# Performance work log

Measured on AMD Instinct MI355X. Metric: run time of the kernel, lower is better.

## Reference

```python
import jax, jax.numpy as jnp
import numpy as np
from jax import lax

B, H, W, C, K, R, CB = 2, 128, 128, 256, 64, 8, 256


def _conv(x, w, b=None, pad=1, lhs_dil=None, groups=1):
    out = lax.conv_general_dilated(x, w, (1, 1), [(pad, pad), (pad, pad)],
                                   lhs_dilation=lhs_dil, feature_group_count=groups,
                                   dimension_numbers=('NCHW', 'OIHW', 'NCHW'))
    return out if b is None else out + b[None, :, None, None]


def _silu(x):
    return x * jax.nn.sigmoid(x)


def _fuse(l0, l1, l2, p1w, p1b, p2w, p3w):
    # proj1: Conv(k=3)+SiLU (BN folded); proj2/proj3: grouped ConvTranspose2d as lhs-dilated grouped convs
    a = _silu(_conv(l0, p1w, p1b))
    b2 = _conv(l1, p2w, pad=2, lhs_dil=(2, 2), groups=CB)  # ConvT(2CB->CB, k4, s2, p1, g=CB)
    b3 = _conv(l2, p3w, pad=5, lhs_dil=(4, 4), groups=CB)  # ConvT(4CB->CB, k8, s4, p2, g=CB)
    return a + b2 + b3


def _corr_map(emb, trk):
    # emb: [H,W,C], trk: [K,C]; cosine-similarity correlation with local argmax radius masking
    e = emb / jnp.maximum(jnp.linalg.norm(emb, axis=-1, keepdims=True), 1e-12)
    t = trk / jnp.maximum(jnp.linalg.norm(trk, axis=-1, keepdims=True), 1e-12)
    y = jnp.maximum(jnp.einsum('hwc,kc->khw', e, t), 0.0)  # torch.where(y>0, y, 0)
    idx = jnp.argmax(y.reshape(K, -1), axis=1)             # first max, like torch.nonzero(...)[0]
    ai, aj = idx // W, idx % W
    rows = jnp.arange(H)[None, :, None]
    cols = jnp.arange(W)[None, None, :]
    m = ((rows >= (ai[:, None, None] - R)) & (rows < (ai[:, None, None] + R)) &
         (cols >= (aj[:, None, None] - R)) & (cols < (aj[:, None, None] + R)))
    s = jnp.sum(y * m, axis=0)
    return s / jnp.max(s)


def setup_inputs():
    key = jax.random.key(0)
    ks = jax.random.split(key, 32)
    r = lambda i, shp, s=0.02: jax.random.normal(ks[i], shp, jnp.float32) * s
    z = lambda n: jnp.zeros((n,), jnp.float32)
    return dict(
        id_embeding=jax.random.normal(ks[0], (B, H, W, C), jnp.float32),
        tracklets=jax.random.normal(ks[1], (B, K, C), jnp.float32),
        l0=jax.random.normal(ks[2], (B, CB, H, W), jnp.float32),
        l1=jax.random.normal(ks[3], (B, 2 * CB, H // 2, W // 2), jnp.float32),
        l2=jax.random.normal(ks[4], (B, 4 * CB, H // 4, W // 4), jnp.float32),
        b_p1w=r(5, (CB, CB, 3, 3)), b_p1b=z(CB),
        b_p2w=r(6, (CB, 2, 4, 4)), b_p3w=r(7, (CB, 4, 8, 8)),
        b_c1w=r(8, (CB, CB, 3, 3)), b_c1b=z(CB),
        b_c2w=r(9, (4, CB, 3, 3)), b_c2b=z(4),
        h_p1w=r(10, (CB, CB, 3, 3)), h_p1b=z(CB),
        h_p2w=r(11, (CB, 2, 4, 4)), h_p3w=r(12, (CB, 4, 8, 8)),
        h_c1aw=r(13, (CB, 1, 3, 3), 0.1), h_c1ab=z(CB),
        h_c1bw=r(14, (1, CB, 3, 3)), h_c1bb=z(1),
        h_c2aw=r(15, (CB, CB, 3, 3)), h_c2ab=z(CB),
        h_c2bw=r(16, (CB, CB, 3, 3)), h_c2bb=z(CB),
        h_c2cw=r(17, (1, CB, 3, 3)), h_c2cb=z(1),
    )


def reference(id_embeding, tracklets, l0, l1, l2,
              b_p1w, b_p1b, b_p2w, b_p3w, b_c1w, b_c1b, b_c2w, b_c2b,
              h_p1w, h_p1b, h_p2w, h_p3w,
              h_c1aw, h_c1ab, h_c1bw, h_c1bb,
              h_c2aw, h_c2ab, h_c2bw, h_c2bb, h_c2cw, h_c2cb):
    # correlation map per batch -> x_F [B,1,H,W]
    x_F = jax.vmap(_corr_map)(id_embeding, tracklets)[:, None]
    # recheck_Box head
    xd_box = _fuse(l0, l1, l2, b_p1w, b_p1b, b_p2w, b_p3w)
    xb = _silu(_conv(xd_box, b_c1w, b_c1b))
    siambox = jnp.transpose(_conv(xb, b_c2w, b_c2b), (0, 2, 3, 1))  # [B,H,W,4]
    # recheck_heatmap head
    xd_hm = _fuse(l0, l1, l2, h_p1w, h_p1b, h_p2w, h_p3w)
    xf = _conv(_silu(_conv(x_F, h_c1aw, h_c1ab)), h_c1bw, h_c1bb)   # [B,1,H,W]
    t = xf * xd_hm                                                  # broadcast over CB channels
    t = _silu(_conv(t, h_c2aw, h_c2ab))
    t = _silu(_conv(t, h_c2bw, h_c2bb))
    hmmap = jax.nn.sigmoid(_conv(t, h_c2cw, h_c2cb))                # [B,1,H,W]
    return (hmmap, siambox)
```

## Files before the change

kernel.cpp:

```cpp
#include <hip/hip_runtime.h>
#include <math.h>

#define HH 128
#define WW 128
#define HWSZ 16384
#define CC 256
#define KK 64
#define BB 2

typedef __bf16 bf16x8_t __attribute__((ext_vector_type(8)));
typedef float  f32x4_t  __attribute__((ext_vector_type(4)));

__device__ __forceinline__ float silu_f(float v) { return v / (1.f + expf(-v)); }
__device__ __forceinline__ float sigm_f(float v) { return 1.f / (1.f + expf(-v)); }

__device__ __forceinline__ float b2f(unsigned short u) {
    union { unsigned int i; float f; } x; x.i = ((unsigned int)u) << 16; return x.f;
}
__device__ __forceinline__ unsigned short f2b(float f) {
    union { float f; unsigned int i; } x; x.f = f;
    unsigned int r = x.i + 0x7FFFu + ((x.i >> 16) & 1u);
    return (unsigned short)(r >> 16);
}
__device__ __forceinline__ float u2f(unsigned int u) {
    union { unsigned int i; float f; } x; x.i = u; return x.f;
}

__global__ __launch_bounds__(256) void cvt_nhwc_kernel(const float* __restrict__ in,
                                                       unsigned short* __restrict__ out) {
    __shared__ float T[32][128];
    const int tid = threadIdx.x;
    const int y = blockIdx.x & 127;
    const int b = blockIdx.x >> 7;
    const float* inb = in + (size_t)b * CC * HWSZ + y * 128;
    unsigned short* outb = out + ((size_t)b * HWSZ + (size_t)y * 128) * CC;

    for (int c0 = 0; c0 < CC; c0 += 32) {
        __syncthreads();
        {
            int cl = tid >> 3;
            int xq = tid & 7;
            const float4* src = (const float4*)(inb + (size_t)(c0 + cl) * HWSZ);
            float4* dst = (float4*)&T[cl][0];
            #pragma unroll
            for (int j = 0; j < 4; j++) dst[xq * 4 + j] = src[xq * 4 + j];
        }
        __syncthreads();
        {
            int x = tid & 127, ch = tid >> 7;
            union { unsigned short u[16]; uint4 v[2]; } pk;
            #pragma unroll
            for (int j = 0; j < 16; j++) pk.u[j] = f2b(T[ch * 16 + j][x]);
            uint4* dst = (uint4*)&outb[(size_t)x * CC + c0 + ch * 16];
            dst[0] = pk.v[0];
            dst[1] = pk.v[1];
        }
    }
}

#define WTSZ (9 * 8 * 256 * 32)
__global__ __launch_bounds__(256) void wprep5_kernel(const float* __restrict__ w0,
                                                     const float* __restrict__ w1,
                                                     const float* __restrict__ w2,
                                                     const float* __restrict__ w3,
                                                     const float* __restrict__ w4,
                                                     unsigned short* __restrict__ wtbase) {
    const float* ws[5] = {w0, w1, w2, w3, w4};
    int set = blockIdx.y;
    const float* w = ws[set];
    int idx = blockIdx.x * 256 + threadIdx.x;
    int e   = idx & 7;
    int co  = (idx >> 3) & 255;
    int g   = (idx >> 11) & 3;
    int v   = idx >> 13;
    int cb  = v / 9;
    int t   = v - cb * 9;
    wtbase[(size_t)set * WTSZ + idx] = f2b(w[((size_t)co * 256 + cb * 32 + g * 8 + e) * 9 + t]);
}

#define EPAD 260
__global__ __launch_bounds__(256) void ycorr_kernel(const float* __restrict__ emb,
                                                    const float* __restrict__ trk,
                                                    float* __restrict__ y) {
    __shared__ __align__(16) float E[64 * EPAD];
    __shared__ __align__(16) float T[64 * EPAD];
    __shared__ float SE[64];
    __shared__ float ST[64];

    const int tid = threadIdx.x;
    const int b   = blockIdx.y;
    const int hw0 = blockIdx.x * 64;

    const float4* esrc = (const float4*)(emb + ((size_t)b * HWSZ + hw0) * CC);
    #pragma unroll
    for (int i = 0; i < 16; i++) {
        int q  = tid + i * 256;
        int px = q >> 6, c4 = q & 63;
        *(float4*)&E[px * EPAD + c4 * 4] = esrc[(size_t)px * 64 + c4];
    }
    const float4* tsrc = (const float4*)(trk + (size_t)b * KK * CC);
    #pragma unroll
    for (int i = 0; i < 16; i++) {
        int q = tid + i * 256;
        int k = q >> 6, c4 = q & 63;
        *(float4*)&T[k * EPAD + c4 * 4] = tsrc[(size_t)k * 64 + c4];
    }
    __syncthreads();

    if (tid < 64) {
        float ss = 0.f;
        const float4* ep = (const float4*)&E[tid * EPAD];
        #pragma unroll 8
        for (int c4 = 0; c4 < 64; c4++) {
            float4 v = ep[c4];
            ss += v.x * v.x + v.y * v.y + v.z * v.z + v.w * v.w;
        }
        SE[tid] = 1.f / fmaxf(sqrtf(ss), 1e-12f);
    } else if (tid < 128) {
        float ss = 0.f;
        const float4* tp = (const float4*)&T[(tid - 64) * EPAD];
        #pragma unroll 8
        for (int c4 = 0; c4 < 64; c4++) {
            float4 v = tp[c4];
            ss += v.x * v.x + v.y * v.y + v.z * v.z + v.w * v.w;
        }
        ST[tid - 64] = 1.f / fmaxf(sqrtf(ss), 1e-12f);
    }
    __syncthreads();

    const int pg = tid & 15;
    const int kg = tid >> 4;

    float acc[4][4];
    #pragma unroll
    for (int jp = 0; jp < 4; jp++)
        #pragma unroll
        for (int jk = 0; jk < 4; jk++) acc[jp][jk] = 0.f;

    const float* Ep[4];
    const float* Tp[4];
    #pragma unroll
    for (int jp = 0; jp < 4; jp++) Ep[jp] = &E[(jp * 16 + pg) * EPAD];
    #pragma unroll
    for (int jk = 0; jk < 4; jk++) Tp[jk] = &T[(jk * 16 + kg) * EPAD];

    #pragma unroll 2
    for (int c4 = 0; c4 < 64; ++c4) {
        float4 e[4], t[4];
        #pragma unroll
        for (int jp = 0; jp < 4; jp++) e[jp] = *(const float4*)(Ep[jp] + c4 * 4);
        #pragma unroll
        for (int jk = 0; jk < 4; jk++) t[jk] = *(const float4*)(Tp[jk] + c4 * 4);
        #define DOT4(a, t) (fmaf(a.w, t.w, fmaf(a.z, t.z, fmaf(a.y, t.y, a.x * t.x))))
        #pragma unroll
        for (int jp = 0; jp < 4; jp++)
            #pragma unroll
            for (int jk = 0; jk < 4; jk++)
                acc[jp][jk] += DOT4(e[jp], t[jk]);
        #undef DOT4
    }

    #pragma unroll
    for (int jp = 0; jp < 4; jp++) {
        int px = jp * 16 + pg;
        float se = SE[px];
        #pragma unroll
        for (int jk = 0; jk < 4; jk++) {
            int k = jk * 16 + kg;
            y[((size_t)b * KK + k) * HWSZ + hw0 + px] = fmaxf(acc[jp][jk], 0.f) * se * ST[k];
        }
    }
}

__global__ __launch_bounds__(256) void argmax_kernel(const float* __restrict__ y,
                                                     int* __restrict__ idxout,
                                                     unsigned int* __restrict__ umax) {
    int bk = blockIdx.x;
    int t = threadIdx.x;
    if (bk == 0 && t < BB) umax[t] = 0u;
    const float* p = y + (size_t)bk * HWSZ;
    float best = -1.f; int bi = 1 << 30;
    for (int i = t; i < HWSZ; i += 256) {
        float v = p[i];
        if (v > best) { best = v; bi = i; }
    }
    __shared__ float sv[256];
    __shared__ int   si[256];
    sv[t] = best; si[t] = bi;
    __syncthreads();
    for (int s = 128; s > 0; s >>= 1) {
        if (t < s) {
            float v2 = sv[t + s]; int i2 = si[t + s];
            if (v2 > sv[t] || (v2 == sv[t] && i2 < si[t])) { sv[t] = v2; si[t] = i2; }
        }
        __syncthreads();
    }
    if (t == 0) idxout[bk] = si[0];
}

__global__ __launch_bounds__(256) void smap_kernel(const float* __restrict__ y,
                                                   const int* __restrict__ idx,
                                                   float* __restrict__ s,
                                                   unsigned int* __restrict__ umax) {
    int b  = blockIdx.y;
    int hw = blockIdx.x * 256 + threadIdx.x;
    int h  = hw >> 7, w = hw & 127;
    __shared__ int ai[KK], aj[KK];
    if (threadIdx.x < KK) {
        int v = idx[b * KK + threadIdx.x];
        ai[threadIdx.x] = v >> 7;
        aj[threadIdx.x] = v & 127;
    }
    __syncthreads();
    const float* yb = y + (size_t)b * KK * HWSZ;
    float acc = 0.f;
    #pragma unroll 8
    for (int k = 0; k < KK; k++) {
        float v = yb[(size_t)k * HWSZ + hw];
        bool in = (h >= ai[k] - 8) && (h < ai[k] + 8) && (w >= aj[k] - 8) && (w < aj[k] + 8);
        acc += in ? v : 0.f;
    }
    s[(size_t)b * HWSZ + hw] = acc;

    __shared__ float sm[256];
    sm[threadIdx.x] = acc;
    __syncthreads();
    for (int st = 128; st > 0; st >>= 1) {
        if (threadIdx.x < st) sm[threadIdx.x] = fmaxf(sm[threadIdx.x], sm[threadIdx.x + st]);
        __syncthreads();
    }
    if (threadIdx.x == 0) {
        union { float f; unsigned int i; } x; x.f = sm[0];
        atomicMax(&umax[b], x.i);
    }
}

__global__ __launch_bounds__(256) void deconv_kernel(const float* __restrict__ l1,
                                                     const float* __restrict__ l2,
                                                     const float* __restrict__ w2,
                                                     const float* __restrict__ w3,
                                                     unsigned short* __restrict__ out) {
    __shared__ float L1[2][64][64];
    __shared__ float L2[4][32][32];

    const int tid = threadIdx.x;
    const int g   = blockIdx.x & 255;
    const int b   = blockIdx.x >> 8;

    const float4* l1b = (const float4*)(l1 + ((size_t)b * 2 * CC + 2 * g) * 4096);
    float4* L1p = (float4*)&L1[0][0][0];
    #pragma unroll
    for (int i = 0; i < 8; i++) L1p[tid + i * 256] = l1b[tid + i * 256];
    const float4* l2b = (const float4*)(l2 + ((size_t)b * 4 * CC + 4 * g) * 1024);
    float4* L2p = (float4*)&L2[0][0][0];
    #pragma unroll
    for (int i = 0; i < 4; i++) L2p[tid + i * 256] = l2b[tid + i * 256];

    const int x    = tid & 127;
    const int ytop = tid >> 7;
    const float* w2g = w2 + (size_t)g * 32;
    const float* w3g = w3 + (size_t)g * 256;

    const int pxo = x & 1, pyo = ytop & 1;
    const int mx0 = (x + pxo - 2) >> 1;
    const int dy2 = (ytop + pyo - 2) >> 1;
    const bool nok0 = (unsigned)mx0 < 64u;
    const bool nok1 = (unsigned)(mx0 + 1) < 64u;
    const int nc0 = mx0 & 63, nc1 = (mx0 + 1) & 63;
    float W2[2][2][2];
    #pragma unroll
    for (int ci = 0; ci < 2; ci++)
        #pragma unroll
        for (int a = 0; a < 2; a++)
            #pragma unroll
            for (int c = 0; c < 2; c++)
                W2[ci][a][c] = w2g[ci * 16 + (pyo + 2 * a) * 4 + (pxo + 2 * c)];

    const int px3 = (5 - (x & 3)) & 3;
    const int n30 = (x + px3 - 5) >> 2;
    const bool n3ok0 = (unsigned)n30 < 32u;
    const bool n3ok1 = (unsigned)(n30 + 1) < 32u;
    const int n3c0 = n30 & 31, n3c1 = (n30 + 1) & 31;
    int dy3[2];
    float W3[2][4][2][2];
    #pragma unroll
    for (int ph = 0; ph < 2; ph++) {
        int py3 = (5 - ((ytop + 2 * ph) & 3)) & 3;
        dy3[ph] = (2 * ph + ytop + py3 - 5) >> 2;
        #pragma unroll
        for (int ci = 0; ci < 4; ci++)
            #pragma unroll
            for (int a = 0; a < 2; a++)
                #pragma unroll
                for (int c = 0; c < 2; c++)
                    W3[ph][ci][a][c] = w3g[ci * 64 + (py3 + 4 * a) * 8 + (px3 + 4 * c)];
    }

    __syncthreads();

    unsigned short* outb = out + ((size_t)b * CC + g) * HWSZ;

    #pragma unroll 2
    for (int ii = 0; ii < 32; ++ii) {
        #pragma unroll
        for (int ph = 0; ph < 2; ph++) {
            const int i = 2 * ii + ph;
            float acc = 0.f;
            {
                const int m0 = i + dy2;
                #pragma unroll
                for (int a = 0; a < 2; a++) {
                    int m = m0 + a;
                    bool mok = (unsigned)m < 64u;
                    int mc = m & 63;
                    #pragma unroll
                    for (int ci = 0; ci < 2; ci++) {
                        float v0 = (mok && nok0) ? L1[ci][mc][nc0] : 0.f;
                        float v1 = (mok && nok1) ? L1[ci][mc][nc1] : 0.f;
                        acc = fmaf(W2[ci][a][0], v0, acc);
                        acc = fmaf(W2[ci][a][1], v1, acc);
                    }
                }
            }
            {
                const int m0 = ii + dy3[ph];
                #pragma unroll
                for (int a = 0; a < 2; a++) {
                    int m = m0 + a;
                    bool mok = (unsigned)m < 32u;
                    int mc = m & 31;
                    #pragma unroll
                    for (int ci = 0; ci < 4; ci++) {
                        float v0 = (mok && n3ok0) ? L2[ci][mc][n3c0] : 0.f;
                        float v1 = (mok && n3ok1) ? L2[ci][mc][n3c1] : 0.f;
                        acc = fmaf(W3[ph][ci][a][0], v0, acc);
                        acc = fmaf(W3[ph][ci][a][1], v1, acc);
                    }
                }
            }
            outb[(size_t)i * 256 + tid] = f2b(acc);
        }
    }
}

template <int ADDB, int MULF>
__global__ __launch_bounds__(256, 2) void conv_mfma_kernel(
    const unsigned short* __restrict__ in,
    const unsigned short* __restrict__ wt,
    const float* __restrict__ bias,
    const unsigned short* __restrict__ addb,
    const float* __restrict__ xf,
    unsigned short* __restrict__ out)
{
    __shared__ __align__(16) unsigned short Alds[2][3 * 130 * 32];

    const int tid  = threadIdx.x;
    const int lane = tid & 63;
    const int wv   = tid >> 6;
    const int wco  = wv >> 1;
    const int wpx  = wv & 1;
    const int l15  = lane & 15;
    const int kg   = lane >> 4;

    const int l   = (blockIdx.x & 7) * 64 + (blockIdx.x >> 3);
    const int y0  = l >> 2;
    const int co0 = ((l >> 1) & 1) * 128;
    const int b   = l & 1;

    const unsigned short* inb = in + (size_t)b * HWSZ * CC;
    const float* xfb = MULF ? (xf + (size_t)b * HWSZ) : nullptr;
    const unsigned short* wp = wt + (size_t)kg * 2048 + (size_t)(co0 + wco * 64 + l15) * 8;

    int ach[3][4];
    #pragma unroll
    for (int tl = 0; tl < 3; tl++)
        #pragma unroll
        for (int f = 0; f < 4; f++) {
            int px = wpx * 64 + f * 16 + l15 + tl;
            ach[tl][f] = (px * 4 + (kg ^ ((px >> 1) & 3))) * 8;
        }

    f32x4_t acc[4][4];
    #pragma unroll
    for (int i = 0; i < 4; i++)
        #pragma unroll
        for (int j = 0; j < 4; j++)
            acc[i][j] = (f32x4_t){0.f, 0.f, 0.f, 0.f};

    if (tid < 48) {
        int q4 = tid & 3;
        int hp = (tid >> 2) & 1;
        int r  = (tid >> 3) % 3;
        int bi = tid / 24;
        int px = hp ? 129 : 0;
        int chunk = (r * 130 + px) * 4 + (q4 ^ ((px >> 1) & 3));
        *reinterpret_cast<uint4*>(&Alds[bi][chunk * 8]) = make_uint4(0u, 0u, 0u, 0u);
    }

    uint4 streg[6];
    float sxf[6];

    auto load_A = [&](int cb) {
        #pragma unroll
        for (int i = 0; i < 6; i++) {
            int q   = tid + i * 256;
            int q4  = q & 3;
            int pxi = (q >> 2) & 127;
            int r   = q >> 9;
            int gy  = y0 - 1 + r;
            uint4 v = make_uint4(0u, 0u, 0u, 0u);
            float fxv = 0.f;
            if ((unsigned)gy < 128u) {
                v = *reinterpret_cast<const uint4*>(
                        inb + ((size_t)(gy * 128 + pxi)) * CC + cb * 32 + q4 * 8);
                if (MULF) fxv = xfb[gy * 128 + pxi];
            }
            streg[i] = v;
            if (MULF) sxf[i] = fxv;
        }
    };
    auto write_A = [&](int bufi) {
        #pragma unroll
        for (int i = 0; i < 6; i++) {
            int q   = tid + i * 256;
            int q4  = q & 3;
            int pxi = (q >> 2) & 127;
            int r   = q >> 9;
            int px  = pxi + 1;
            int chunk = (r * 130 + px) * 4 + (q4 ^ ((px >> 1) & 3));
            uint4 v = streg[i];
            if (MULF) {
                union { unsigned short u[8]; uint4 w; } pk;
                pk.w = v;
                float fm = sxf[i];
                #pragma unroll
                for (int e = 0; e < 8; e++) pk.u[e] = f2b(b2f(pk.u[e]) * fm);
                v = pk.w;
            }
            *reinterpret_cast<uint4*>(&Alds[bufi][chunk * 8]) = v;
        }
    };

    load_A(0);
    write_A(0);

    bf16x8_t W[3][4], P[2][4];
    #pragma unroll
    for (int f = 0; f < 4; f++) W[0][f] = *reinterpret_cast<const bf16x8_t*>(wp + f * 128);
    #pragma unroll
    for (int f = 0; f < 4; f++) W[1][f] = *reinterpret_cast<const bf16x8_t*>(wp + 8192 + f * 128);

    __syncthreads();
    #pragma unroll
    for (int f = 0; f < 4; f++)
        P[0][f] = *reinterpret_cast<const bf16x8_t*>(&Alds[0][ach[0][f]]);

    for (int cb = 0; cb < 8; ++cb) {
        const int bufi = cb & 1;
        if (cb + 1 < 8) load_A(cb + 1);
        const unsigned short* wcb = wp + (size_t)cb * 73728;
        #pragma unroll
        for (int t = 0; t < 9; ++t) {
            if (cb < 7 || t < 7) {
                #pragma unroll
                for (int f = 0; f < 4; f++)
                    W[(t + 2) % 3][f] = *reinterpret_cast<const bf16x8_t*>(
                        wcb + (t + 2) * 8192 + f * 128);
            }
            if (t < 8) {
                const int aoff = ((t + 1) / 3) * 4160;
                #pragma unroll
                for (int f = 0; f < 4; f++)
                    P[(t + 1) & 1][f] = *reinterpret_cast<const bf16x8_t*>(
                        &Alds[bufi][aoff + ach[(t + 1) % 3][f]]);
            }
            __builtin_amdgcn_sched_barrier(0);
            #pragma unroll
            for (int cf = 0; cf < 4; cf++)
                #pragma unroll
                for (int pf = 0; pf < 4; pf++)
                    acc[cf][pf] = __builtin_amdgcn_mfma_f32_16x16x32_bf16(
                        W[t % 3][cf], P[t & 1][pf], acc[cf][pf], 0, 0, 0);
        }
        if (cb + 1 < 8) write_A(bufi ^ 1);
        __syncthreads();
        if (cb + 1 < 8) {
            #pragma unroll
            for (int f = 0; f < 4; f++)
                P[0][f] = *reinterpret_cast<const bf16x8_t*>(&Alds[(cb + 1) & 1][ach[0][f]]);
        }
    }

    size_t outB = ((size_t)b * HWSZ + (size_t)y0 * 128) * CC;
    #pragma unroll
    for (int cf = 0; cf < 4; cf++) {
        int co = co0 + wco * 64 + cf * 16 + kg * 4;
        float bs0 = bias[co], bs1 = bias[co + 1], bs2 = bias[co + 2], bs3 = bias[co + 3];
        #pragma unroll
        for (int pf = 0; pf < 4; pf++) {
            int x = wpx * 64 + pf * 16 + l15;
            float v0 = silu_f(acc[cf][pf][0] + bs0);
            float v1 = silu_f(acc[cf][pf][1] + bs1);
            float v2 = silu_f(acc[cf][pf][2] + bs2);
            float v3 = silu_f(acc[cf][pf][3] + bs3);
            if (ADDB) {
                size_t ab = ((size_t)b * CC + co) * HWSZ + (size_t)y0 * 128 + x;
                v0 += b2f(addb[ab]);
                v1 += b2f(addb[ab + HWSZ]);
                v2 += b2f(addb[ab + 2 * HWSZ]);
                v3 += b2f(addb[ab + 3 * HWSZ]);
            }
            union { unsigned short u[4]; uint2 v; } pk;
            pk.u[0] = f2b(v0); pk.u[1] = f2b(v1); pk.u[2] = f2b(v2); pk.u[3] = f2b(v3);
            *reinterpret_cast<uint2*>(&out[outB + (size_t)x * CC + co]) = pk.v;
        }
    }
}

__global__ __launch_bounds__(256) void conv_c1a_kernel(const float* __restrict__ s,
                                                       const unsigned int* __restrict__ umax,
                                                       const float* __restrict__ w,
                                                       const float* __restrict__ bias,
                                                       unsigned short* __restrict__ out) {
    __shared__ float W[2304];
    __shared__ float S[3][34];

    const int tid = threadIdx.x;
    const int idx = blockIdx.x;
    const int b   = idx >> 9;
    const int seg = idx & 511;
    const int y   = seg >> 2;
    const int x0  = (seg & 3) * 32;

    for (int i = tid; i < 2304; i += 256) W[i] = w[i];
    if (tid < 102) {
        int r = tid / 34, xx = tid - r * 34;
        int gy = y - 1 + r, gx = x0 - 1 + xx;
        S[r][xx] = ((unsigned)gy < 128u && (unsigned)gx < 128u)
                       ? s[(size_t)b * HWSZ + gy * 128 + gx] : 0.f;
    }
    __syncthreads();

    const float im = 1.f / u2f(umax[b]);
    const int cog = tid >> 5;
    const int px  = tid & 31;

    float sv[9];
    #pragma unroll
    for (int r = 0; r < 3; r++)
        #pragma unroll
        for (int d = 0; d < 3; d++)
            sv[r * 3 + d] = S[r][px + d];

    unsigned short* op =
        &out[((size_t)b * HWSZ + (size_t)y * 128 + x0 + px) * CC + cog * 32];
    #pragma unroll
    for (int q = 0; q < 4; q++) {
        union { unsigned short u[8]; uint4 v; } pk;
        #pragma unroll
        for (int j = 0; j < 8; j++) {
            int co = cog * 32 + q * 8 + j;
            float a = 0.f;
            #pragma unroll
            for (int t = 0; t < 9; t++) a = fmaf(W[co * 9 + t], sv[t], a);
            pk.u[j] = f2b(silu_f(a * im + bias[co]));
        }
        *reinterpret_cast<uint4*>(op + q * 8) = pk.v;
    }
}

template <int COUT, int MODE>
__global__ __launch_bounds__(256) void small_conv_kernel(
    const unsigned short* __restrict__ in,
    const float* __restrict__ w,
    const float* __restrict__ bias,
    float* __restrict__ out)
{
    __shared__ float WL[COUT * 9 * 32 * 12];

    const int tid = threadIdx.x;
    for (int i = tid; i < COUT * 2304; i += 256) {
        int e = i & 7;
        int g = (i >> 3) & 31;
        int rest = i >> 8;
        int t = rest % 9;
        int co = rest / 9;
        WL[((co * 9 + t) * 32 + g) * 12 + e] = w[((size_t)co * 256 + g * 8 + e) * 9 + t];
    }
    __syncthreads();

    const int lane = tid & 63;
    const int wv   = tid >> 6;
    const int c32  = lane & 31;
    const int ps   = lane >> 5;
    const int grp  = blockIdx.x * 4 + wv;
    const int base = grp * 4;
    const int b    = base >> 14;
    const int pix  = base & (HWSZ - 1);
    const int y    = pix >> 7;
    const int x0   = pix & 127;
    const int p0x  = x0 + 2 * ps;

    const unsigned short* inb = in + (size_t)b * HWSZ * CC;

    uint4 d[3][4];
    #pragma unroll
    for (int r = 0; r < 3; r++) {
        int gy = y - 1 + r;
        #pragma unroll
        for (int cx = 0; cx < 4; cx++) {
            int gx = p0x - 1 + cx;
            uint4 v = make_uint4(0u, 0u, 0u, 0u);
            if ((unsigned)gy < 128u && (unsigned)gx < 128u)
                v = *reinterpret_cast<const uint4*>(
                        inb + ((size_t)(gy * 128 + gx)) * CC + c32 * 8);
            d[r][cx] = v;
        }
    }

    float acc[2][COUT];
    #pragma unroll
    for (int p = 0; p < 2; p++)
        #pragma unroll
        for (int c = 0; c < COUT; c++) acc[p][c] = 0.f;

    #pragma unroll
    for (int r = 0; r < 3; r++) {
        float f[4][8];
        #pragma unroll
        for (int cx = 0; cx < 4; cx++) {
            union { unsigned short u[8]; uint4 v; } pk;
            pk.v = d[r][cx];
            #pragma unroll
            for (int e = 0; e < 8; e++) f[cx][e] = b2f(pk.u[e]);
        }
        #pragma unroll
        for (int dx = 0; dx < 3; dx++) {
            #pragma unroll
            for (int co = 0; co < COUT; co++) {
                int bse = ((co * 9 + r * 3 + dx) * 32 + c32) * 12;
                float4 wa = *(const float4*)&WL[bse];
                float4 wb = *(const float4*)&WL[bse + 4];
                #pragma unroll
                for (int p = 0; p < 2; p++) {
                    const float* ff = f[dx + p];
                    float a = acc[p][co];
                    a = fmaf(ff[0], wa.x, a); a = fmaf(ff[1], wa.y, a);
                    a = fmaf(ff[2], wa.z, a); a = fmaf(ff[3], wa.w, a);
                    a = fmaf(ff[4], wb.x, a); a = fmaf(ff[5], wb.y, a);
                    a = fmaf(ff[6], wb.z, a); a = fmaf(ff[7], wb.w, a);
                    acc[p][co] = a;
                }
            }
        }
    }

    #pragma unroll
    for (int m = 1; m <= 16; m <<= 1)
        #pragma unroll
        for (int p = 0; p < 2; p++)
            #pragma unroll
            for (int co = 0; co < COUT; co++)
                acc[p][co] += __shfl_xor(acc[p][co], m);

    if (c32 == 0) {
        #pragma unroll
        for (int p = 0; p < 2; p++) {
            size_t pixidx = (size_t)base + 2 * ps + p;
            if (MODE == 0) {
                ((float4*)out)[pixidx] = make_float4(
                    acc[p][0] + bias[0],
                    acc[p][COUT > 1 ? 1 : 0] + bias[COUT > 1 ? 1 : 0],
                    acc[p][COUT > 2 ? 2 : 0] + bias[COUT > 2 ? 2 : 0],
                    acc[p][COUT > 3 ? 3 : 0] + bias[COUT > 3 ? 3 : 0]);
            } else if (MODE == 1) {
                out[pixidx] = acc[p][0] + bias[0];
            } else {
                out[pixidx] = sigm_f(acc[p][0] + bias[0]);
            }
        }
    }
}

extern "C" void kernel_launch(void* const* d_in, const int* in_sizes, int n_in,
                              void* d_out, int out_size, void* d_ws, size_t ws_size,
                              hipStream_t stream) {
    const float* emb    = (const float*)d_in[0];
    const float* trk    = (const float*)d_in[1];
    const float* l0     = (const float*)d_in[2];
    const float* l1     = (const float*)d_in[3];
    const float* l2     = (const float*)d_in[4];
    const float* b_p1w  = (const float*)d_in[5];
    const float* b_p1b  = (const float*)d_in[6];
    const float* b_p2w  = (const float*)d_in[7];
    const float* b_p3w  = (const float*)d_in[8];
    const float* b_c1w  = (const float*)d_in[9];
    const float* b_c1b  = (const float*)d_in[10];
    const float* b_c2w  = (const float*)d_in[11];
    const float* b_c2b  = (const float*)d_in[12];
    const float* h_p1w  = (const float*)d_in[13];
    const float* h_p1b  = (const float*)d_in[14];
    const float* h_p2w  = (const float*)d_in[15];
    const float* h_p3w  = (const float*)d_in[16];
    const float* h_c1aw = (const float*)d_in[17];
    const float* h_c1ab = (const float*)d_in[18];
    const float* h_c1bw = (const float*)d_in[19];
    const float* h_c1bb = (const float*)d_in[20];
    const float* h_c2aw = (const float*)d_in[21];
    const float* h_c2ab = (const float*)d_in[22];
    const float* h_c2bw = (const float*)d_in[23];
    const float* h_c2bb = (const float*)d_in[24];
    const float* h_c2cw = (const float*)d_in[25];
    const float* h_c2cb = (const float*)d_in[26];

    float* outp = (float*)d_out;

    const size_t ACT = (size_t)BB * CC * HWSZ;
    const size_t WT  = (size_t)WTSZ;

    unsigned short* l0nh = (unsigned short*)d_ws;
    unsigned short* wt0  = l0nh + ACT;
    unsigned short* wt1  = wt0 + WT;
    unsigned short* wt2  = wt1 + WT;
    unsigned short* wt3  = wt2 + WT;
    unsigned short* wt4  = wt3 + WT;
    unsigned short* Db   = wt4 + WT;
    unsigned short* X1   = Db + ACT;
    unsigned short* X2   = X1 + ACT;
    float* sbuf   = (float*)(X2 + ACT);
    float* xfb    = sbuf + (size_t)BB * HWSZ;
    unsigned int* umax = (unsigned int*)(xfb + (size_t)BB * HWSZ);
    int*   idxb   = (int*)(umax + 2);
    float* ybuf   = (float*)X1;

    cvt_nhwc_kernel<<<BB * 128, 256, 0, stream>>>(l0, l0nh);
    wprep5_kernel<<<dim3((unsigned)(WT / 256), 5), 256, 0, stream>>>(
        b_p1w, b_c1w, h_p1w, h_c2aw, h_c2bw, wt0);

    ycorr_kernel<<<dim3(256, BB), 256, 0, stream>>>(emb, trk, ybuf);
    argmax_kernel<<<BB * KK, 256, 0, stream>>>(ybuf, idxb, umax);
    smap_kernel<<<dim3(64, BB), 256, 0, stream>>>(ybuf, idxb, sbuf, umax);

    deconv_kernel<<<BB * CC, 256, 0, stream>>>(l1, l2, b_p2w, b_p3w, Db);
    conv_mfma_kernel<1, 0><<<512, 256, 0, stream>>>(l0nh, wt0, b_p1b, Db, nullptr, X1);
    conv_mfma_kernel<0, 0><<<512, 256, 0, stream>>>(X1, wt1, b_c1b, nullptr, nullptr, X2);
    small_conv_kernel<4, 0><<<2048, 256, 0, stream>>>(X2, b_c2w, b_c2b, outp + BB * HWSZ);

    deconv_kernel<<<BB * CC, 256, 0, stream>>>(l1, l2, h_p2w, h_p3w, Db);
    conv_mfma_kernel<1, 0><<<512, 256, 0, stream>>>(l0nh, wt2, h_p1b, Db, nullptr, X1);
    conv_c1a_kernel<<<1024, 256, 0, stream>>>(sbuf, umax, h_c1aw, h_c1ab, X2);
    small_conv_kernel<1, 1><<<2048, 256, 0, stream>>>(X2, h_c1bw, h_c1bb, xfb);
    conv_mfma_kernel<0, 1><<<512, 256, 0, stream>>>(X1, wt3, h_c2ab, nullptr, xfb, Db);
    conv_mfma_kernel<0, 0><<<512, 256, 0, stream>>>(Db, wt4, h_c2bb, nullptr, nullptr, X1);
    small_conv_kernel<1, 2><<<2048, 256, 0, stream>>>(X1, h_c2cw, h_c2cb, outp);
}
```

Baseline: 409.5 us.

## Merge both heads' deconv and proj1 conv into dual-head kernels sharing loaded inputs

The deconv kernel now computes both the box and heatmap heads' transposed convolutions from a single shared-memory load of l1/l2. The first 3x3 MFMA conv for both heads is merged into one 1024-block launch that reads l0 once and picks weights by head. This drops two launches, avoids reloading inputs, and gives the merged conv a larger grid. It needs an extra activation buffer in the workspace, and a fallback path keeps the old sequence when the workspace is too small.

```diff
diff --git a/kernel.cpp b/kernel.cpp
--- a/kernel.cpp
+++ b/kernel.cpp
@@ -235,11 +235,15 @@
     }
 }
 
+template <int HEADS>
 __global__ __launch_bounds__(256) void deconv_kernel(const float* __restrict__ l1,
                                                      const float* __restrict__ l2,
-                                                     const float* __restrict__ w2,
-                                                     const float* __restrict__ w3,
-                                                     unsigned short* __restrict__ out) {
+                                                     const float* __restrict__ w2a,
+                                                     const float* __restrict__ w3a,
+                                                     const float* __restrict__ w2b,
+                                                     const float* __restrict__ w3b,
+                                                     unsigned short* __restrict__ outA,
+                                                     unsigned short* __restrict__ outB) {
     __shared__ float L1[2][64][64];
     __shared__ float L2[4][32][32];
 
@@ -258,8 +262,6 @@
 
     const int x    = tid & 127;
     const int ytop = tid >> 7;
-    const float* w2g = w2 + (size_t)g * 32;
-    const float* w3g = w3 + (size_t)g * 256;
 
     const int pxo = x & 1, pyo = ytop & 1;
     const int mx0 = (x + pxo - 2) >> 1;
@@ -267,93 +269,107 @@
     const bool nok0 = (unsigned)mx0 < 64u;
     const bool nok1 = (unsigned)(mx0 + 1) < 64u;
     const int nc0 = mx0 & 63, nc1 = (mx0 + 1) & 63;
-    float W2[2][2][2];
-    #pragma unroll
-    for (int ci = 0; ci < 2; ci++)
-        #pragma unroll
-        for (int a = 0; a < 2; a++)
-            #pragma unroll
-            for (int c = 0; c < 2; c++)
-                W2[ci][a][c] = w2g[ci * 16 + (pyo + 2 * a) * 4 + (pxo + 2 * c)];
 
     const int px3 = (5 - (x & 3)) & 3;
     const int n30 = (x + px3 - 5) >> 2;
     const bool n3ok0 = (unsigned)n30 < 32u;
     const bool n3ok1 = (unsigned)(n30 + 1) < 32u;
     const int n3c0 = n30 & 31, n3c1 = (n30 + 1) & 31;
-    int dy3[2];
-    float W3[2][4][2][2];
+    int dy3[2], py3v[2];
     #pragma unroll
     for (int ph = 0; ph < 2; ph++) {
         int py3 = (5 - ((ytop + 2 * ph) & 3)) & 3;
+        py3v[ph] = py3;
         dy3[ph] = (2 * ph + ytop + py3 - 5) >> 2;
-        #pragma unroll
-        for (int ci = 0; ci < 4; ci++)
+    }
+
+    __syncthreads();
+
+    const float* w2s[2] = {w2a, w2b};
+    const float* w3s[2] = {w3a, w3b};
+    unsigned short* outs[2] = {outA, outB};
+
+    #pragma unroll 1
+    for (int hd = 0; hd < HEADS; ++hd) {
+        const float* w2g = w2s[hd] + (size_t)g * 32;
+        const float* w3g = w3s[hd] + (size_t)g * 256;
+
+        float W2[2][2][2];
+        #pragma unroll
+        for (int ci = 0; ci < 2; ci++)
             #pragma unroll
             for (int a = 0; a < 2; a++)
                 #pragma unroll
                 for (int c = 0; c < 2; c++)
-                    W3[ph][ci][a][c] = w3g[ci * 64 + (py3 + 4 * a) * 8 + (px3 + 4 * c)];
-    }
-
-    __syncthreads();
-
-    unsigned short* outb = out + ((size_t)b * CC + g) * HWSZ;
-
-    #pragma unroll 2
-    for (int ii = 0; ii < 32; ++ii) {
-        #pragma unroll
-        for (int ph = 0; ph < 2; ph++) {
-            const int i = 2 * ii + ph;
-            float acc = 0.f;
-            {
-                const int m0 = i + dy2;
+                    W2[ci][a][c] = w2g[ci * 16 + (pyo + 2 * a) * 4 + (pxo + 2 * c)];
+        float W3[2][4][2][2];
+        #pragma unroll
+        for (int ph = 0; ph < 2; ph++)
+            #pragma unroll
+            for (int ci = 0; ci < 4; ci++)
                 #pragma unroll
-                for (int a = 0; a < 2; a++) {
-                    int m = m0 + a;
-                    bool mok = (unsigned)m < 64u;
-                    int mc = m & 63;
+                for (int a = 0; a < 2; a++)
                     #pragma unroll
-                    for (int ci = 0; ci < 2; ci++) {
-                        float v0 = (mok && nok0) ? L1[ci][mc][nc0] : 0.f;
-                        float v1 = (mok && nok1) ? L1[ci][mc][nc1] : 0.f;
-                        acc = fmaf(W2[ci][a][0], v0, acc);
-                        acc = fmaf(W2[ci][a][1], v1, acc);
+                    for (int c = 0; c < 2; c++)
+                        W3[ph][ci][a][c] = w3g[ci * 64 + (py3v[ph] + 4 * a) * 8 + (px3 + 4 * c)];
+
+        unsigned short* outb = outs[hd] + ((size_t)b * CC + g) * HWSZ;
+
+        #pragma unroll 2
+        for (int ii = 0; ii < 32; ++ii) {
+            #pragma unroll
+            for (int ph = 0; ph < 2; ph++) {
+                const int i = 2 * ii + ph;
+                float acc = 0.f;
+                {
+                    const int m0 = i + dy2;
+                    #pragma unroll
+                    for (int a = 0; a < 2; a++) {
+                        int m = m0 + a;
+                        bool mok = (unsigned)m < 64u;
+                        int mc = m & 63;
+                        #pragma unroll
+                        for (int ci = 0; ci < 2; ci++) {
+                            float v0 = (mok && nok0) ? L1[ci][mc][nc0] : 0.f;
+                            float v1 = (mok && nok1) ? L1[ci][mc][nc1] : 0.f;
+                            acc = fmaf(W2[ci][a][0], v0, acc);
+                            acc = fmaf(W2[ci][a][1], v1, acc);
+                        }
                     }
                 }
-            }
-            {
-                const int m0 = ii + dy3[ph];
-                #pragma unroll
-                for (int a = 0; a < 2; a++) {
-                    int m = m0 + a;
-                    bool mok = (unsigned)m < 32u;
-                    int mc = m & 31;
+                {
+                    const int m0 = ii + dy3[ph];
                     #pragma unroll
-                    for (int ci = 0; ci < 4; ci++) {
-                        float v0 = (mok && n3ok0) ? L2[ci][mc][n3c0] : 0.f;
-                        float v1 = (mok && n3ok1) ? L2[ci][mc][n3c1] : 0.f;
-                        acc = fmaf(W3[ph][ci][a][0], v0, acc);
-                        acc = fmaf(W3[ph][ci][a][1], v1, acc);
+                    for (int a = 0; a < 2; a++) {
+                        int m = m0 + a;
+                        bool mok = (unsigned)m < 32u;
+                        int mc = m & 31;
+                        #pragma unroll
+                        for (int ci = 0; ci < 4; ci++) {
+                            float v0 = (mok && n3ok0) ? L2[ci][mc][n3c0] : 0.f;
+                            float v1 = (mok && n3ok1) ? L2[ci][mc][n3c1] : 0.f;
+                            acc = fmaf(W3[ph][ci][a][0], v0, acc);
+                            acc = fmaf(W3[ph][ci][a][1], v1, acc);
+                        }
                     }
                 }
+                outb[(size_t)i * 256 + tid] = f2b(acc);
             }
-            outb[(size_t)i * 256 + tid] = f2b(acc);
         }
     }
 }
 
 template <int ADDB, int MULF>
-__global__ __launch_bounds__(256, 2) void conv_mfma_kernel(
+__device__ __forceinline__ void conv_mfma_body(
+    int y0, int co0, int b,
     const unsigned short* __restrict__ in,
     const unsigned short* __restrict__ wt,
     const float* __restrict__ bias,
     const unsigned short* __restrict__ addb,
     const float* __restrict__ xf,
-    unsigned short* __restrict__ out)
+    unsigned short* __restrict__ out,
+    unsigned short (*Alds)[3 * 130 * 32])
 {
-    __shared__ __align__(16) unsigned short Alds[2][3 * 130 * 32];
-
     const int tid  = threadIdx.x;
     const int lane = tid & 63;
     const int wv   = tid >> 6;
@@ -361,11 +377,6 @@
     const int wpx  = wv & 1;
     const int l15  = lane & 15;
     const int kg   = lane >> 4;
-
-    const int l   = (blockIdx.x & 7) * 64 + (blockIdx.x >> 3);
-    const int y0  = l >> 2;
-    const int co0 = ((l >> 1) & 1) * 128;
-    const int b   = l & 1;
 
     const unsigned short* inb = in + (size_t)b * HWSZ * CC;
     const float* xfb = MULF ? (xf + (size_t)b * HWSZ) : nullptr;
@@ -515,6 +526,50 @@
             *reinterpret_cast<uint2*>(&out[outB + (size_t)x * CC + co]) = pk.v;
         }
     }
+}
+
+template <int ADDB, int MULF>
+__global__ __launch_bounds__(256, 2) void conv_mfma_kernel(
+    const unsigned short* __restrict__ in,
+    const unsigned short* __restrict__ wt,
+    const float* __restrict__ bias,
+    const unsigned short* __restrict__ addb,
+    const float* __restrict__ xf,
+    unsigned short* __restrict__ out)
+{
+    __shared__ __align__(16) unsigned short Alds[2][3 * 130 * 32];
+    const int l   = (blockIdx.x & 7) * 64 + (blockIdx.x >> 3);
+    const int y0  = l >> 2;
+    const int co0 = ((l >> 1) & 1) * 128;
+    const int b   = l & 1;
+    conv_mfma_body<ADDB, MULF>(y0, co0, b, in, wt, bias, addb, xf, out, Alds);
+}
+
+__global__ __launch_bounds__(256, 2) void conv_mfma_dual_kernel(
+    const unsigned short* __restrict__ in,
+    const unsigned short* __restrict__ wt2set,
+    const float* __restrict__ biasB,
+    const float* __restrict__ biasH,
+    const unsigned short* __restrict__ addbB,
+    const unsigned short* __restrict__ addbH,
+    unsigned short* __restrict__ outB,
+    unsigned short* __restrict__ outH)
+{
+    __shared__ __align__(16) unsigned short Alds[2][3 * 130 * 32];
+    const int l    = (blockIdx.x & 7) * 128 + (blockIdx.x >> 3);
+    const int y0   = l >> 3;
+    const int c3   = l & 7;
+    const int head = c3 >> 2;
+    const int co0  = ((c3 >> 1) & 1) * 128;
+    const int b    = c3 & 1;
+    conv_mfma_body<1, 0>(y0, co0, b,
+                         in,
+                         wt2set + (size_t)head * WTSZ,
+                         head ? biasH : biasB,
+                         head ? addbH : addbB,
+                         nullptr,
+                         head ? outH : outB,
+                         Alds);
 }
 
 __global__ __launch_bounds__(256) void conv_c1a_kernel(const float* __restrict__ s,
@@ -717,40 +772,66 @@
 
     const size_t ACT = (size_t)BB * CC * HWSZ;
     const size_t WT  = (size_t)WTSZ;
+    const size_t SMALLS = 131400;
 
     unsigned short* l0nh = (unsigned short*)d_ws;
-    unsigned short* wt0  = l0nh + ACT;
-    unsigned short* wt1  = wt0 + WT;
-    unsigned short* wt2  = wt1 + WT;
-    unsigned short* wt3  = wt2 + WT;
-    unsigned short* wt4  = wt3 + WT;
-    unsigned short* Db   = wt4 + WT;
-    unsigned short* X1   = Db + ACT;
-    unsigned short* X2   = X1 + ACT;
-    float* sbuf   = (float*)(X2 + ACT);
+    unsigned short* wtP  = l0nh + ACT;
+    unsigned short* bufA = wtP + 5 * WT;
+    unsigned short* bufB = bufA + ACT;
+    unsigned short* bufC = bufB + ACT;
+    float* sbuf   = (float*)(bufC + ACT);
     float* xfb    = sbuf + (size_t)BB * HWSZ;
     unsigned int* umax = (unsigned int*)(xfb + (size_t)BB * HWSZ);
     int*   idxb   = (int*)(umax + 2);
-    float* ybuf   = (float*)X1;
+    unsigned short* bufD = bufC + ACT + SMALLS;
+    float* ybuf   = (float*)bufB;
+
+    const size_t NEED = (size_t)(bufD + ACT - l0nh) * sizeof(unsigned short);
+    const bool fast = ws_size >= NEED;
 
     cvt_nhwc_kernel<<<BB * 128, 256, 0, stream>>>(l0, l0nh);
     wprep5_kernel<<<dim3((unsigned)(WT / 256), 5), 256, 0, stream>>>(
-        b_p1w, b_c1w, h_p1w, h_c2aw, h_c2bw, wt0);
+        b_p1w, h_p1w, b_c1w, h_c2aw, h_c2bw, wtP);
 
     ycorr_kernel<<<dim3(256, BB), 256, 0, stream>>>(emb, trk, ybuf);
     argmax_kernel<<<BB * KK, 256, 0, stream>>>(ybuf, idxb, umax);
     smap_kernel<<<dim3(64, BB), 256, 0, stream>>>(ybuf, idxb, sbuf, umax);
 
-    deconv_kernel<<<BB * CC, 256, 0, stream>>>(l1, l2, b_p2w, b_p3w, Db);
-    conv_mfma_kernel<1, 0><<<512, 256, 0, stream>>>(l0nh, wt0, b_p1b, Db, nullptr, X1);
-    conv_mfma_kernel<0, 0><<<512, 256, 0, stream>>>(X1, wt1, b_c1b, nullptr, nullptr, X2);
-    small_conv_kernel<4, 0><<<2048, 256, 0, stream>>>(X2, b_c2w, b_c2b, outp + BB * HWSZ);
-
-    deconv_kernel<<<BB * CC, 256, 0, stream>>>(l1, l2, h_p2w, h_p3w, Db);
-    conv_mfma_kernel<1, 0><<<512, 256, 0, stream>>>(l0nh, wt2, h_p1b, Db, nullptr, X1);
-    conv_c1a_kernel<<<1024, 256, 0, stream>>>(sbuf, umax, h_c1aw, h_c1ab, X2);
-    small_conv_kernel<1, 1><<<2048, 256, 0, stream>>>(X2, h_c1bw, h_c1bb, xfb);
-    conv_mfma_kernel<0, 1><<<512, 256, 0, stream>>>(X1, wt3, h_c2ab, nullptr, xfb, Db);
-    conv_mfma_kernel<0, 0><<<512, 256, 0, stream>>>(Db, wt4, h_c2bb, nullptr, nullptr, X1);
-    small_conv_kernel<1, 2><<<2048, 256, 0, stream>>>(X1, h_c2cw, h_c2cb, outp);
-}
+    if (fast) {
+        deconv_kernel<2><<<BB * CC, 256, 0, stream>>>(l1, l2, b_p2w, b_p3w, h_p2w, h_p3w,
+                                                      bufA, bufD);
+        conv_mfma_dual_kernel<<<1024, 256, 0, stream>>>(l0nh, wtP, b_p1b, h_p1b,
+                                                        bufA, bufD, bufB, bufC);
+        conv_mfma_kernel<0, 0><<<512, 256, 0, stream>>>(bufB, wtP + 2 * WT, b_c1b,
+                                                        nullptr, nullptr, bufA);
+        small_conv_kernel<4, 0><<<2048, 256, 0, stream>>>(bufA, b_c2w, b_c2b,
+                                                          outp + BB * HWSZ);
+        conv_c1a_kernel<<<1024, 256, 0, stream>>>(sbuf, umax, h_c1aw, h_c1ab, bufB);
+        small_conv_kernel<1, 1><<<2048, 256, 0, stream>>>(bufB, h_c1bw, h_c1bb, xfb);
+        conv_mfma_kernel<0, 1><<<512, 256, 0, stream>>>(bufC, wtP + 3 * WT, h_c2ab,
+                                                        nullptr, xfb, bufA);
+        conv_mfma_kernel<0, 0><<<512, 256, 0, stream>>>(bufA, wtP + 4 * WT, h_c2bb,
+                                                        nullptr, nullptr, bufB);
+        small_conv_kernel<1, 2><<<2048, 256, 0, stream>>>(bufB, h_c2cw, h_c2cb, outp);
+    } else {
+        deconv_kernel<1><<<BB * CC, 256, 0, stream>>>(l1, l2, b_p2w, b_p3w,
+                                                      nullptr, nullptr, bufA, nullptr);
+        conv_mfma_kernel<1, 0><<<512, 256, 0, stream>>>(l0nh, wtP, b_p1b, bufA,
+                                                        nullptr, bufB);
+        conv_mfma_kernel<0, 0><<<512, 256, 0, stream>>>(bufB, wtP + 2 * WT, b_c1b,
+                                                        nullptr, nullptr, bufC);
+        small_conv_kernel<4, 0><<<2048, 256, 0, stream>>>(bufC, b_c2w, b_c2b,
+                                                          outp + BB * HWSZ);
+        deconv_kernel<1><<<BB * CC, 256, 0, stream>>>(l1, l2, h_p2w, h_p3w,
+                                                      nullptr, nullptr, bufA, nullptr);
+        conv_mfma_kernel<1, 0><<<512, 256, 0, stream>>>(l0nh, wtP + 1 * WT, h_p1b, bufA,
+                                                        nullptr, bufB);
+        conv_c1a_kernel<<<1024, 256, 0, stream>>>(sbuf, umax, h_c1aw, h_c1ab, bufC);
+        small_conv_kernel<1, 1><<<2048, 256, 0, stream>>>(bufC, h_c1bw, h_c1bb, xfb);
+        conv_mfma_kernel<0, 1><<<512, 256, 0, stream>>>(bufB, wtP + 3 * WT, h_c2ab,
+                                                        nullptr, xfb, bufA);
+        conv_mfma_kernel<0, 0><<<512, 256, 0, stream>>>(bufA, wtP + 4 * WT, h_c2bb,
+                                                        nullptr, nullptr, bufC);
+        small_conv_kernel<1, 2><<<2048, 256, 0, stream>>>(bufC, h_c2cw, h_c2cb, outp);
+    }
+}
```

Result: faster. 400.3 us (-2.3%).
